# Performance work log

Hardware: AMD Instinct MI355X
Metric: run time of the kernel (lower is better)

The kernel has to match this reference:

```python
import jax, jax.numpy as jnp
import numpy as np

OFFSET = 1
NUM_ENTITY = 128

def setup_inputs() -> dict:
    key = jax.random.key(0)
    ks = jax.random.split(key, 8)
    B, L, D = 32, 2048, 1024
    M, E, S = 256, NUM_ENTITY, 128
    H, P = 2048, 512
    return {
        "sequence_output": jax.random.normal(ks[0], (B, L, D), dtype=jnp.float32),
        "mention_pos": jax.random.randint(ks[1], (B, M), 0, L - 2),
        "mention2entity": jnp.sort(jax.random.randint(ks[2], (B, M), 0, E), axis=-1),
        "sent_pos": jax.random.randint(ks[3], (B, S), 0, L - 2),
        "fc1_w": jax.random.normal(ks[4], (D, H), dtype=jnp.float32) * 0.02,
        "fc1_b": jnp.zeros((H,), dtype=jnp.float32),
        "fc2_w": jax.random.normal(ks[5], (H, P), dtype=jnp.float32) * 0.02,
        "fc2_b": jnp.zeros((P,), dtype=jnp.float32),
    }

def _segment_logsumexp(x, seg):
    # x: [M, D] mention embeddings, seg: [M] entity ids -> [E, D]
    m = jax.ops.segment_max(x, seg, num_segments=NUM_ENTITY)           # [E, D]
    m_safe = jnp.where(jnp.isfinite(m), m, 0.0)
    s = jax.ops.segment_sum(jnp.exp(x - m_safe[seg]), seg, num_segments=NUM_ENTITY)
    cnt = jax.ops.segment_sum(jnp.ones((x.shape[0],), x.dtype), seg, num_segments=NUM_ENTITY)
    s_safe = jnp.where(cnt[:, None] > 0, s, 1.0)
    lse = jnp.log(s_safe) + m_safe
    # entities with no mentions stay zero (torch.zeros init in original)
    return jnp.where(cnt[:, None] > 0, lse, 0.0)

def reference(sequence_output, mention_pos, mention2entity, sent_pos, fc1_w, fc1_b, fc2_w, fc2_b):
    # gather mention start-token states (offset = +1 as in self.offset)
    mention_embed = jnp.take_along_axis(
        sequence_output, (mention_pos + OFFSET)[:, :, None], axis=1)  # [B, M, D]
    sent_embed = jnp.take_along_axis(
        sequence_output, (sent_pos + OFFSET)[:, :, None], axis=1)     # [B, S, D]
    entity_embed = jax.vmap(_segment_logsumexp)(mention_embed, mention2entity)  # [B, E, D]
    nodes = jnp.concatenate([mention_embed, entity_embed, sent_embed], axis=1)  # [B, M+E+S, D]
    # projection(): fc1 then fc2 (no nonlinearity, as in the original)
    h = jnp.einsum('bnd,dh->bnh', nodes, fc1_w) + fc1_b
    return jnp.einsum('bnh,hp->bnp', h, fc2_w) + fc2_b
```

## Files before the change

kernel.cpp:

```cpp
#include <hip/hip_runtime.h>
#include <cstdint>

#define DEV __device__ __forceinline__

typedef __attribute__((ext_vector_type(8))) short short8;
typedef __attribute__((ext_vector_type(4))) float f32x4;

DEV unsigned short f2bf(float f) {
    uint32_t u = __builtin_bit_cast(uint32_t, f);
    u += 0x7fffu + ((u >> 16) & 1u);
    return (unsigned short)(u >> 16);
}

DEV uint32_t cvtpk(float a, float b) {
    uint32_t r;
    asm("v_cvt_pk_bf16_f32 %0, %1, %2" : "=v"(r) : "v"(a), "v"(b));
    return r;
}

DEV uint2 pack4(float4 v) {
    uint2 o;
    o.x = cvtpk(v.x, v.y);
    o.y = cvtpk(v.z, v.w);
    return o;
}

DEV void async_copy16(void* lds, const void* g) {
    __builtin_amdgcn_global_load_lds(
        (const __attribute__((address_space(1))) void*)g,
        (__attribute__((address_space(3))) void*)lds, 16, 0, 0);
}

template <int KLEN, int KSTR, int N>
DEV void gemm_body_part(const unsigned short* __restrict__ A,
                        const unsigned short* __restrict__ Bt,
                        float* __restrict__ P,
                        int Mtot, int rowblk, int colblk, int zidx,
                        unsigned short* Al, unsigned short* Bl) {
    int t = threadIdx.x;
    int lane = t & 63, w = t >> 6;
    int wm = w >> 1, wn = w & 1;
    int row0 = rowblk * 128, col0 = colblk * 128;
    size_t kbase = (size_t)zidx * KLEN;
    f32x4 acc[4][4] = {};

    int rifc = lane >> 2;
    int koff = (lane & 3) * 8;
    int c0 = 2 * w, c1 = 2 * w + 1;

    const unsigned short* Abase = A + (size_t)row0 * KSTR + kbase + koff;
    const unsigned short* Bbase = Bt + (size_t)col0 * KSTR + kbase + koff;

    for (int kt = 0; kt < KLEN / 32; ++kt) {
        int k0 = kt * 32;
        __syncthreads();
        async_copy16(&Al[c0 * 512], Abase + (size_t)(c0 * 16 + rifc) * KSTR + k0);
        async_copy16(&Al[c1 * 512], Abase + (size_t)(c1 * 16 + rifc) * KSTR + k0);
        async_copy16(&Bl[c0 * 512], Bbase + (size_t)(c0 * 16 + rifc) * KSTR + k0);
        async_copy16(&Bl[c1 * 512], Bbase + (size_t)(c1 * 16 + rifc) * KSTR + k0);
        __syncthreads();

        int r = lane & 15, kq = lane >> 4;
        short8 a[4], b[4];
        #pragma unroll
        for (int mi = 0; mi < 4; ++mi)
            a[mi] = *reinterpret_cast<const short8*>(&Al[(wm * 64 + mi * 16 + r) * 32 + kq * 8]);
        #pragma unroll
        for (int ni = 0; ni < 4; ++ni)
            b[ni] = *reinterpret_cast<const short8*>(&Bl[(wn * 64 + ni * 16 + r) * 32 + kq * 8]);
        #pragma unroll
        for (int mi = 0; mi < 4; ++mi)
            #pragma unroll
            for (int ni = 0; ni < 4; ++ni)
                acc[mi][ni] = __builtin_amdgcn_mfma_f32_16x16x32_bf16(a[mi], b[ni], acc[mi][ni], 0, 0, 0);
    }

    int r = lane & 15, kq = lane >> 4;
    float* Pz = P + (size_t)zidx * (size_t)N * (size_t)Mtot;
    #pragma unroll
    for (int mi = 0; mi < 4; ++mi)
        #pragma unroll
        for (int ni = 0; ni < 4; ++ni) {
            int col = col0 + wn * 64 + ni * 16 + r;
            #pragma unroll
            for (int j = 0; j < 4; ++j) {
                int row = row0 + wm * 64 + mi * 16 + kq * 4 + j;
                Pz[(size_t)col * Mtot + row] = acc[mi][ni][j];
            }
        }
}

__global__ __launch_bounds__(256) void k_prep(const float* __restrict__ W1,
                                              const float* __restrict__ W2,
                                              const float* __restrict__ b1,
                                              unsigned short* __restrict__ W1c,
                                              unsigned short* __restrict__ W2t,
                                              float* __restrict__ part) {
    __shared__ unsigned short sh[32][33];
    int blk = blockIdx.x, t = threadIdx.x;
    if (blk < 2048) {
        int i = blk * 256 + t;
        float4 v = reinterpret_cast<const float4*>(W1)[i];
        reinterpret_cast<uint2*>(W1c)[i] = pack4(v);
    } else if (blk < 3072) {
        int idx = blk - 2048;
        int h0 = (idx & 63) * 32, p0 = (idx >> 6) * 32;
        int r = t >> 3, c4 = (t & 7) * 4;
        float4 v = *reinterpret_cast<const float4*>(&W2[(size_t)(h0 + r) * 512 + p0 + c4]);
        sh[r][c4 + 0] = f2bf(v.x);
        sh[r][c4 + 1] = f2bf(v.y);
        sh[r][c4 + 2] = f2bf(v.z);
        sh[r][c4 + 3] = f2bf(v.w);
        __syncthreads();
        uint2 o;
        o.x = (uint32_t)sh[c4 + 0][r] | ((uint32_t)sh[c4 + 1][r] << 16);
        o.y = (uint32_t)sh[c4 + 2][r] | ((uint32_t)sh[c4 + 3][r] << 16);
        *reinterpret_cast<uint2*>(&W2t[(size_t)(p0 + r) * 2048 + h0 + c4]) = o;
    } else {
        int hs = blk - 3072;
        float a0 = 0.f, a1 = 0.f;
        #pragma unroll 4
        for (int hh = 0; hh < 32; ++hh) {
            int h = hs * 32 + hh;
            float bb = b1[h];
            a0 += bb * W2[(size_t)h * 512 + t];
            a1 += bb * W2[(size_t)h * 512 + 256 + t];
        }
        part[hs * 512 + t] = a0;
        part[hs * 512 + 256 + t] = a1;
    }
}

__global__ __launch_bounds__(256) void k_mid(const float* __restrict__ seq,
                                             const int* __restrict__ mpos,
                                             const int* __restrict__ m2e,
                                             const unsigned short* __restrict__ W1c,
                                             const unsigned short* __restrict__ W2t,
                                             float* __restrict__ Wpart,
                                             const float* __restrict__ part,
                                             const float* __restrict__ b2,
                                             float* __restrict__ fb,
                                             unsigned short* __restrict__ ent) {
    __shared__ unsigned short Al[128 * 32];
    __shared__ unsigned short Bl[128 * 32];
    __shared__ int sm[256];
    __shared__ int sp[256];
    __shared__ int slo, shi;
    int blk = blockIdx.x, t = threadIdx.x;
    if (blk < 128) {
        gemm_body_part<512, 2048, 512>(W1c, W2t, Wpart, 1024,
                                       (blk >> 2) & 7, blk & 3, blk >> 5, Al, Bl);
    } else if (blk < 130) {
        int p = (blk - 128) * 256 + t;
        float s = b2[p];
        #pragma unroll
        for (int hs = 0; hs < 64; ++hs) s += part[hs * 512 + p];
        fb[p] = s;
    } else {
        int idx = blk - 130;
        int b = idx >> 7, e = idx & 127;
        sm[t] = m2e[b * 256 + t];
        sp[t] = mpos[b * 256 + t] + 1;
        if (t == 0) { slo = 0; shi = 0; }
        __syncthreads();
        if (sm[t] == e && (t == 0 || sm[t - 1] != e)) slo = t;
        if (sm[t] == e && (t == 255 || sm[t + 1] != e)) shi = t + 1;
        __syncthreads();
        int lo = slo, hi = shi;
        float ox, oy, oz, ow;
        if (hi > lo) {
            float s0 = 0.f, s1 = 0.f, s2 = 0.f, s3 = 0.f;
            for (int j = lo; j < hi; ++j) {
                float4 v = *reinterpret_cast<const float4*>(
                    &seq[((size_t)b * 2048 + sp[j]) * 1024 + t * 4]);
                s0 += __expf(v.x); s1 += __expf(v.y);
                s2 += __expf(v.z); s3 += __expf(v.w);
            }
            ox = __logf(s0); oy = __logf(s1);
            oz = __logf(s2); ow = __logf(s3);
        } else {
            ox = oy = oz = ow = 0.f;
        }
        float4 o; o.x = ox; o.y = oy; o.z = oz; o.w = ow;
        *reinterpret_cast<uint2*>(&ent[((size_t)b * 128 + e) * 1024 + t * 4]) = pack4(o);
    }
}

__global__ __launch_bounds__(256) void k_wreduce(const float* __restrict__ P,
                                                 unsigned short* __restrict__ Wt) {
    const size_t SPLIT = 512u * 1024u;
    int i = blockIdx.x * 256 + threadIdx.x;
    float4 a = reinterpret_cast<const float4*>(P)[i];
    float4 b = reinterpret_cast<const float4*>(P + SPLIT)[i];
    float4 c = reinterpret_cast<const float4*>(P + 2 * SPLIT)[i];
    float4 d = reinterpret_cast<const float4*>(P + 3 * SPLIT)[i];
    float4 s;
    s.x = a.x + b.x + c.x + d.x;
    s.y = a.y + b.y + c.y + d.y;
    s.z = a.z + b.z + c.z + d.z;
    s.w = a.w + b.w + c.w + d.w;
    reinterpret_cast<uint2*>(Wt)[i] = pack4(s);
}

__global__ __launch_bounds__(512) void k_gemm_main(const float* __restrict__ seq,
                                                   const int* __restrict__ mpos,
                                                   const int* __restrict__ spos,
                                                   const unsigned short* __restrict__ ent,
                                                   const unsigned short* __restrict__ Wt,
                                                   float* __restrict__ C,
                                                   const float* __restrict__ fb) {
    __shared__ unsigned short Al[128 * 32];
    __shared__ unsigned short Bl[256 * 32];
    int p = blockIdx.x;
    int cpx = gridDim.x >> 3;
    int L = (p & 7) * cpx + (p >> 3);
    int colblk = L & 1;
    int rowblk = L >> 1;

    int t = threadIdx.x;
    int lane = t & 63, w = t >> 6;
    int wm = w >> 2, wn = w & 3;
    int row0 = rowblk * 128, col0 = colblk * 256;
    int b = rowblk >> 2, quad = rowblk & 3;
    f32x4 acc[4][4] = {};

    int rifc = lane >> 2;
    int koff = (lane & 3) * 8;
    int c0 = 2 * w, c1 = 2 * w + 1;
    const unsigned short* Bbase = Wt + (size_t)col0 * 1024 + koff;

    auto compute = [&]() {
        int r = lane & 15, kq = lane >> 4;
        short8 a[4], bfr[4];
        #pragma unroll
        for (int mi = 0; mi < 4; ++mi)
            a[mi] = *reinterpret_cast<const short8*>(&Al[(wm * 64 + mi * 16 + r) * 32 + kq * 8]);
        #pragma unroll
        for (int ni = 0; ni < 4; ++ni)
            bfr[ni] = *reinterpret_cast<const short8*>(&Bl[(wn * 64 + ni * 16 + r) * 32 + kq * 8]);
        #pragma unroll
        for (int mi = 0; mi < 4; ++mi)
            #pragma unroll
            for (int ni = 0; ni < 4; ++ni)
                acc[mi][ni] = __builtin_amdgcn_mfma_f32_16x16x32_bf16(a[mi], bfr[ni], acc[mi][ni], 0, 0, 0);
    };

    auto stageB = [&](int kt) {
        int k0 = kt * 32;
        async_copy16(&Bl[c0 * 512], Bbase + (size_t)(c0 * 16 + rifc) * 1024 + k0);
        async_copy16(&Bl[c1 * 512], Bbase + (size_t)(c1 * 16 + rifc) * 1024 + k0);
    };

    if (quad == 2) {
        const unsigned short* Abase = ent + (size_t)b * 128 * 1024 + koff;
        #pragma unroll 1
        for (int kt = 0; kt < 32; ++kt) {
            int k0 = kt * 32;
            __syncthreads();
            async_copy16(&Al[w * 512], Abase + (size_t)(w * 16 + rifc) * 1024 + k0);
            stageB(kt);
            __syncthreads();
            compute();
        }
    } else {
        int rloc = t >> 2;
        int cof = (t & 3) * 8;
        const float* rp;
        {
            int pos;
            if (quad == 3) pos = spos[b * 128 + rloc] + 1;
            else           pos = mpos[b * 256 + quad * 128 + rloc] + 1;
            rp = seq + ((size_t)b * 2048 + pos) * 1024 + cof;
        }
        float4 va[2];
        auto loadA = [&](int kt, float4* dst) {
            int k0 = kt * 32;
            dst[0] = *reinterpret_cast<const float4*>(rp + k0);
            dst[1] = *reinterpret_cast<const float4*>(rp + k0 + 4);
        };
        auto writeA = [&](const float4* src) {
            *reinterpret_cast<uint2*>(&Al[rloc * 32 + cof])     = pack4(src[0]);
            *reinterpret_cast<uint2*>(&Al[rloc * 32 + cof + 4]) = pack4(src[1]);
        };
        loadA(0, va);
        #pragma unroll 1
        for (int kt = 0; kt < 32; ++kt) {
            __syncthreads();
            writeA(va);
            stageB(kt);
            __syncthreads();
            float4 vn[2];
            if (kt < 31) loadA(kt + 1, vn);
            compute();
            va[0] = vn[0]; va[1] = vn[1];
        }
    }

    int r = lane & 15, kq = lane >> 4;
    #pragma unroll
    for (int mi = 0; mi < 4; ++mi)
        #pragma unroll
        for (int ni = 0; ni < 4; ++ni) {
            int col = col0 + wn * 64 + ni * 16 + r;
            float bv = fb[col];
            #pragma unroll
            for (int j = 0; j < 4; ++j) {
                int row = row0 + wm * 64 + mi * 16 + kq * 4 + j;
                C[(size_t)row * 512 + col] = acc[mi][ni][j] + bv;
            }
        }
}


extern "C" void kernel_launch(void* const* d_in, const int* in_sizes, int n_in,
                              void* d_out, int out_size, void* d_ws, size_t ws_size,
                              hipStream_t stream) {
    const float* seq  = (const float*)d_in[0];
    const int*   mpos = (const int*)d_in[1];
    const int*   m2e  = (const int*)d_in[2];
    const int*   spos = (const int*)d_in[3];
    const float* W1   = (const float*)d_in[4];
    const float* b1   = (const float*)d_in[5];
    const float* W2   = (const float*)d_in[6];
    const float* b2   = (const float*)d_in[7];
    float* out = (float*)d_out;

    char* ws = (char*)d_ws;
    unsigned short* W1c   = (unsigned short*)(ws);
    unsigned short* W2t   = (unsigned short*)(ws + (4u << 20));
    unsigned short* Wt    = (unsigned short*)(ws + (6u << 20));
    float*          Wpart = (float*)(ws + (8u << 20));
    float*          part  = (float*)(ws + (16u << 20));
    float*          fb    = (float*)(ws + (16u << 20) + (1u << 18));
    unsigned short* ent   = (unsigned short*)(ws + (24u << 20));

    k_prep<<<3136, 256, 0, stream>>>(W1, W2, b1, W1c, W2t, part);
    k_mid<<<4226, 256, 0, stream>>>(seq, mpos, m2e, W1c, W2t, Wpart, part, b2, fb, ent);
    k_wreduce<<<512, 256, 0, stream>>>(Wpart, Wt);
    k_gemm_main<<<256, 512, 0, stream>>>(seq, mpos, spos, ent, Wt, out, fb);
}
```

Measured before the change: 68.58 us.

## Pre-gather node rows to bf16 in prep kernel and simplify main GEMM

Measured after the change: 71.02 us. 1.04x slower.

```diff
diff --git a/kernel.cpp b/kernel.cpp
--- a/kernel.cpp
+++ b/kernel.cpp
@@ -93,12 +93,25 @@
 __global__ __launch_bounds__(256) void k_prep(const float* __restrict__ W1,
                                               const float* __restrict__ W2,
                                               const float* __restrict__ b1,
+                                              const float* __restrict__ seq,
+                                              const int* __restrict__ mpos,
+                                              const int* __restrict__ spos,
                                               unsigned short* __restrict__ W1c,
                                               unsigned short* __restrict__ W2t,
-                                              float* __restrict__ part) {
+                                              float* __restrict__ part,
+                                              unsigned short* __restrict__ nodes) {
     __shared__ unsigned short sh[32][33];
     int blk = blockIdx.x, t = threadIdx.x;
-    if (blk < 2048) {
+    if (blk >= 3136) {
+        int idx = blk - 3136;
+        int b = idx / 384, i = idx % 384;
+        int node, pos;
+        if (i < 256) { node = i;        pos = mpos[b * 256 + i] + 1; }
+        else         { node = i + 128;  pos = spos[b * 128 + (i - 256)] + 1; }
+        float4 v = *reinterpret_cast<const float4*>(
+            &seq[((size_t)b * 2048 + pos) * 1024 + t * 4]);
+        *reinterpret_cast<uint2*>(&nodes[((size_t)b * 512 + node) * 1024 + t * 4]) = pack4(v);
+    } else if (blk < 2048) {
         int i = blk * 256 + t;
         float4 v = reinterpret_cast<const float4*>(W1)[i];
         reinterpret_cast<uint2*>(W1c)[i] = pack4(v);
@@ -140,7 +153,7 @@
                                              const float* __restrict__ part,
                                              const float* __restrict__ b2,
                                              float* __restrict__ fb,
-                                             unsigned short* __restrict__ ent) {
+                                             unsigned short* __restrict__ nodes) {
     __shared__ unsigned short Al[128 * 32];
     __shared__ unsigned short Bl[128 * 32];
     __shared__ int sm[256];
@@ -182,7 +195,7 @@
             ox = oy = oz = ow = 0.f;
         }
         float4 o; o.x = ox; o.y = oy; o.z = oz; o.w = ow;
-        *reinterpret_cast<uint2*>(&ent[((size_t)b * 128 + e) * 1024 + t * 4]) = pack4(o);
+        *reinterpret_cast<uint2*>(&nodes[((size_t)b * 512 + 256 + e) * 1024 + t * 4]) = pack4(o);
     }
 }
 
@@ -202,98 +215,54 @@
     reinterpret_cast<uint2*>(Wt)[i] = pack4(s);
 }
 
-__global__ __launch_bounds__(512) void k_gemm_main(const float* __restrict__ seq,
-                                                   const int* __restrict__ mpos,
-                                                   const int* __restrict__ spos,
-                                                   const unsigned short* __restrict__ ent,
-                                                   const unsigned short* __restrict__ Wt,
+__global__ __launch_bounds__(256) void k_gemm_main(const unsigned short* __restrict__ A,
+                                                   const unsigned short* __restrict__ Bt,
                                                    float* __restrict__ C,
                                                    const float* __restrict__ fb) {
     __shared__ unsigned short Al[128 * 32];
-    __shared__ unsigned short Bl[256 * 32];
+    __shared__ unsigned short Bl[128 * 32];
     int p = blockIdx.x;
     int cpx = gridDim.x >> 3;
     int L = (p & 7) * cpx + (p >> 3);
-    int colblk = L & 1;
-    int rowblk = L >> 1;
+    int colblk = L & 3;
+    int rowblk = L >> 2;
 
     int t = threadIdx.x;
     int lane = t & 63, w = t >> 6;
-    int wm = w >> 2, wn = w & 3;
-    int row0 = rowblk * 128, col0 = colblk * 256;
-    int b = rowblk >> 2, quad = rowblk & 3;
+    int wm = w >> 1, wn = w & 1;
+    int row0 = rowblk * 128, col0 = colblk * 128;
     f32x4 acc[4][4] = {};
 
     int rifc = lane >> 2;
     int koff = (lane & 3) * 8;
     int c0 = 2 * w, c1 = 2 * w + 1;
-    const unsigned short* Bbase = Wt + (size_t)col0 * 1024 + koff;
-
-    auto compute = [&]() {
+
+    const unsigned short* Abase = A + (size_t)row0 * 1024 + koff;
+    const unsigned short* Bbase = Bt + (size_t)col0 * 1024 + koff;
+
+    #pragma unroll 1
+    for (int kt = 0; kt < 32; ++kt) {
+        int k0 = kt * 32;
+        __syncthreads();
+        async_copy16(&Al[c0 * 512], Abase + (size_t)(c0 * 16 + rifc) * 1024 + k0);
+        async_copy16(&Al[c1 * 512], Abase + (size_t)(c1 * 16 + rifc) * 1024 + k0);
+        async_copy16(&Bl[c0 * 512], Bbase + (size_t)(c0 * 16 + rifc) * 1024 + k0);
+        async_copy16(&Bl[c1 * 512], Bbase + (size_t)(c1 * 16 + rifc) * 1024 + k0);
+        __syncthreads();
+
         int r = lane & 15, kq = lane >> 4;
-        short8 a[4], bfr[4];
+        short8 a[4], b[4];
         #pragma unroll
         for (int mi = 0; mi < 4; ++mi)
             a[mi] = *reinterpret_cast<const short8*>(&Al[(wm * 64 + mi * 16 + r) * 32 + kq * 8]);
         #pragma unroll
         for (int ni = 0; ni < 4; ++ni)
-            bfr[ni] = *reinterpret_cast<const short8*>(&Bl[(wn * 64 + ni * 16 + r) * 32 + kq * 8]);
+            b[ni] = *reinterpret_cast<const short8*>(&Bl[(wn * 64 + ni * 16 + r) * 32 + kq * 8]);
         #pragma unroll
         for (int mi = 0; mi < 4; ++mi)
             #pragma unroll
             for (int ni = 0; ni < 4; ++ni)
-                acc[mi][ni] = __builtin_amdgcn_mfma_f32_16x16x32_bf16(a[mi], bfr[ni], acc[mi][ni], 0, 0, 0);
-    };
-
-    auto stageB = [&](int kt) {
-        int k0 = kt * 32;
-        async_copy16(&Bl[c0 * 512], Bbase + (size_t)(c0 * 16 + rifc) * 1024 + k0);
-        async_copy16(&Bl[c1 * 512], Bbase + (size_t)(c1 * 16 + rifc) * 1024 + k0);
-    };
-
-    if (quad == 2) {
-        const unsigned short* Abase = ent + (size_t)b * 128 * 1024 + koff;
-        #pragma unroll 1
-        for (int kt = 0; kt < 32; ++kt) {
-            int k0 = kt * 32;
-            __syncthreads();
-            async_copy16(&Al[w * 512], Abase + (size_t)(w * 16 + rifc) * 1024 + k0);
-            stageB(kt);
-            __syncthreads();
-            compute();
-        }
-    } else {
-        int rloc = t >> 2;
-        int cof = (t & 3) * 8;
-        const float* rp;
-        {
-            int pos;
-            if (quad == 3) pos = spos[b * 128 + rloc] + 1;
-            else           pos = mpos[b * 256 + quad * 128 + rloc] + 1;
-            rp = seq + ((size_t)b * 2048 + pos) * 1024 + cof;
-        }
-        float4 va[2];
-        auto loadA = [&](int kt, float4* dst) {
-            int k0 = kt * 32;
-            dst[0] = *reinterpret_cast<const float4*>(rp + k0);
-            dst[1] = *reinterpret_cast<const float4*>(rp + k0 + 4);
-        };
-        auto writeA = [&](const float4* src) {
-            *reinterpret_cast<uint2*>(&Al[rloc * 32 + cof])     = pack4(src[0]);
-            *reinterpret_cast<uint2*>(&Al[rloc * 32 + cof + 4]) = pack4(src[1]);
-        };
-        loadA(0, va);
-        #pragma unroll 1
-        for (int kt = 0; kt < 32; ++kt) {
-            __syncthreads();
-            writeA(va);
-            stageB(kt);
-            __syncthreads();
-            float4 vn[2];
-            if (kt < 31) loadA(kt + 1, vn);
-            compute();
-            va[0] = vn[0]; va[1] = vn[1];
-        }
+                acc[mi][ni] = __builtin_amdgcn_mfma_f32_16x16x32_bf16(a[mi], b[ni], acc[mi][ni], 0, 0, 0);
     }
 
     int r = lane & 15, kq = lane >> 4;
@@ -332,10 +301,10 @@
     float*          Wpart = (float*)(ws + (8u << 20));
     float*          part  = (float*)(ws + (16u << 20));
     float*          fb    = (float*)(ws + (16u << 20) + (1u << 18));
-    unsigned short* ent   = (unsigned short*)(ws + (24u << 20));
-
-    k_prep<<<3136, 256, 0, stream>>>(W1, W2, b1, W1c, W2t, part);
-    k_mid<<<4226, 256, 0, stream>>>(seq, mpos, m2e, W1c, W2t, Wpart, part, b2, fb, ent);
+    unsigned short* nodes = (unsigned short*)(ws + (24u << 20));
+
+    k_prep<<<15424, 256, 0, stream>>>(W1, W2, b1, seq, mpos, spos, W1c, W2t, part, nodes);
+    k_mid<<<4226, 256, 0, stream>>>(seq, mpos, m2e, W1c, W2t, Wpart, part, b2, fb, nodes);
     k_wreduce<<<512, 256, 0, stream>>>(Wpart, Wt);
-    k_gemm_main<<<256, 512, 0, stream>>>(seq, mpos, spos, ent, Wt, out, fb);
-}
+    k_gemm_main<<<512, 256, 0, stream>>>(nodes, Wt, out, fb);
+}
```
